# Kernel optimization log

Hardware: AMD Instinct MI355X
Metric: run time of the kernel (lower is better)

## Reference

```python
import jax, jax.numpy as jnp
import numpy as np

N_NODES = 50000
NEG_SLOPE = 0.2  # PyG GATConv default leaky_relu slope


def setup_inputs() -> dict:
    key = jax.random.key(0)
    ks = jax.random.split(key, 12)
    N, E, D_IN, H = N_NODES, 1200000, 128, 64
    sd_in = 1.0 / np.sqrt(D_IN)
    sd_h = 1.0 / np.sqrt(H)
    return {
        "x": jax.random.normal(ks[0], (N, D_IN), jnp.float32),
        "src": jax.random.randint(ks[1], (E,), 0, N, jnp.int32),
        "dst": jax.random.randint(ks[2], (E,), 0, N, jnp.int32),
        "W1_src": jax.random.normal(ks[3], (D_IN, H), jnp.float32) * sd_in,
        "W1_dst": jax.random.normal(ks[4], (D_IN, H), jnp.float32) * sd_in,
        "a1_src": jax.random.normal(ks[5], (H,), jnp.float32) * sd_h,
        "a1_dst": jax.random.normal(ks[6], (H,), jnp.float32) * sd_h,
        "b1": jnp.zeros((H,), jnp.float32),
        "W2_src": jax.random.normal(ks[7], (H, H), jnp.float32) * sd_h,
        "W2_dst": jax.random.normal(ks[8], (H, H), jnp.float32) * sd_h,
        "a2_src": jax.random.normal(ks[9], (H,), jnp.float32) * sd_h,
        "a2_dst": jax.random.normal(ks[10], (H,), jnp.float32) * sd_h,
        "b2": jnp.zeros((H,), jnp.float32),
    }


def _gat_layer(x, src, dst, W_src, W_dst, att_src, att_dst, bias):
    N = x.shape[0]
    h_src = x @ W_src            # [N, H] transformed source features
    h_dst = x @ W_dst            # [N, H] transformed destination features
    alpha_src = h_src @ att_src  # [N]
    alpha_dst = h_dst @ att_dst  # [N]
    # edge-wise attention logits (gather), edge j -> i: e = lrelu(a_src[j] + a_dst[i])
    e = jax.nn.leaky_relu(alpha_src[src] + alpha_dst[dst], NEG_SLOPE)  # [E]
    # segment softmax over incoming edges of each destination node
    m = jax.ops.segment_max(e, dst, num_segments=N)          # [N]
    ex = jnp.exp(e - m[dst])                                  # [E]
    denom = jax.ops.segment_sum(ex, dst, num_segments=N)     # [N]
    alpha = ex / denom[dst]                                   # [E]
    # weighted scatter-add aggregation
    msgs = h_src[src] * alpha[:, None]                        # [E, H]
    out = jax.ops.segment_sum(msgs, dst, num_segments=N)     # [N, H]
    return out + bias


def reference(x, src, dst, W1_src, W1_dst, a1_src, a1_dst, b1,
              W2_src, W2_dst, a2_src, a2_dst, b2):
    h = jnp.tanh(_gat_layer(x, src, dst, W1_src, W1_dst, a1_src, a1_dst, b1))
    h = jnp.tanh(_gat_layer(h, src, dst, W2_src, W2_dst, a2_src, a2_dst, b2))
    return h
```

## Files before the change

### kernel.cpp

```cpp
#include <hip/hip_runtime.h>
#include <hip/hip_bf16.h>

#define NEG_SLOPE 0.2f
#define EPB 4096
#define NHB 64
#define NBUK 1024

typedef __attribute__((ext_vector_type(8))) short short8v;
typedef __attribute__((ext_vector_type(4))) float f32x4;

__device__ inline float blo(unsigned u) { return __uint_as_float(u << 16); }
__device__ inline float bhi(unsigned u) { return __uint_as_float(u & 0xffff0000u); }
__device__ inline unsigned short bf16bits(float f) {
    __hip_bfloat16 b = __float2bfloat16(f);
    return *(unsigned short*)&b;
}
__device__ inline unsigned pack2bf(float e, float o) {
    return ((unsigned)bf16bits(o) << 16) | (unsigned)bf16bits(e);
}

template <int K>
__device__ inline void build_wt(unsigned short* __restrict__ Wt,
                                const float* __restrict__ W_src,
                                const float* __restrict__ a_src,
                                const float* __restrict__ W_dst,
                                const float* __restrict__ a_dst, int tid) {
    for (int i = tid; i < 64 * K; i += 256) {
        int k = i >> 6, j = i & 63;
        Wt[j * K + k] = bf16bits(W_src[i]);
    }
    for (int i = tid; i < 2 * K; i += 256) {
        int which = (i >= K) ? 1 : 0;
        int k = i - which * K;
        const float* Wr = (which ? W_dst : W_src) + k * 64;
        const float* av = which ? a_dst : a_src;
        float s = 0.f;
        #pragma unroll
        for (int j = 0; j < 64; ++j) s += Wr[j] * av[j];
        Wt[(64 + which) * K + k] = bf16bits(s);
    }
    for (int i = tid; i < 14 * K; i += 256) Wt[66 * K + i] = 0;
}

__global__ __launch_bounds__(256) void prep(
    const int* __restrict__ dst, int* __restrict__ partials, int E,
    const float* __restrict__ W1_src, const float* __restrict__ a1_src,
    const float* __restrict__ W1_dst, const float* __restrict__ a1_dst,
    const float* __restrict__ W2_src, const float* __restrict__ a2_src,
    const float* __restrict__ W2_dst, const float* __restrict__ a2_dst,
    unsigned short* __restrict__ Wt1, unsigned short* __restrict__ Wt2) {
    __shared__ int lh[NBUK];
    int tid = threadIdx.x, b = blockIdx.x;
    if (b < NHB) {
        for (int s = tid; s < NBUK; s += 256) lh[s] = 0;
        __syncthreads();
        for (int e = b * 256 + tid; e < E; e += NHB * 256)
            atomicAdd(&lh[dst[e] >> 6], 1);
        __syncthreads();
        for (int s = tid; s < NBUK; s += 256)
            partials[b * NBUK + s] = lh[s];
    } else if (b == NHB) {
        build_wt<128>(Wt1, W1_src, a1_src, W1_dst, a1_dst, tid);
    } else {
        build_wt<64>(Wt2, W2_src, a2_src, W2_dst, a2_dst, tid);
    }
}

__global__ __launch_bounds__(256) void scan1024(const int* __restrict__ partials,
                                                int* __restrict__ bucket_base,
                                                int* __restrict__ cursor0) {
    __shared__ int tsum[256];
    int tid = threadIdx.x;
    int4 v = make_int4(0, 0, 0, 0);
    for (int b = 0; b < NHB; ++b) {
        int4 p = *(const int4*)&partials[b * NBUK + 4 * tid];
        v.x += p.x; v.y += p.y; v.z += p.z; v.w += p.w;
    }
    int t = v.x + v.y + v.z + v.w;
    tsum[tid] = t;
    __syncthreads();
    for (int off = 1; off < 256; off <<= 1) {
        int u = (tid >= off) ? tsum[tid - off] : 0;
        __syncthreads();
        tsum[tid] += u;
        __syncthreads();
    }
    int base = tsum[tid] - t;
    bucket_base[4 * tid + 0] = base;
    bucket_base[4 * tid + 1] = base + v.x;
    bucket_base[4 * tid + 2] = base + v.x + v.y;
    bucket_base[4 * tid + 3] = base + v.x + v.y + v.z;
    if (tid == 255) bucket_base[NBUK] = tsum[255];
    *(int4*)&cursor0[4 * tid] = make_int4(0, 0, 0, 0);
}

template <int K, bool INBF16>
__device__ inline void nt_body(int nb, const void* __restrict__ x_,
                               const unsigned short* __restrict__ Wt,
                               unsigned* __restrict__ hb_out,
                               float* __restrict__ alpha_src,
                               float* __restrict__ alpha_dst, int N, int tid) {
    int wid = tid >> 6, l = tid & 63;
    int rowbase = (nb * 4 + wid) * 16;
    if (rowbase >= N) return;
    int jcol = l & 15, kg = (l >> 4) * 8;

    int r = rowbase + jcol;
    if (r >= N) r = N - 1;
    const float*          xr32 = (const float*)x_ + (size_t)r * K + kg;
    const unsigned short* xr16 = (const unsigned short*)x_ + (size_t)r * K + kg;

    f32x4 acc[5];
    #pragma unroll
    for (int t = 0; t < 5; ++t) acc[t] = (f32x4){0.f, 0.f, 0.f, 0.f};

    #pragma unroll
    for (int kt = 0; kt < K / 32; ++kt) {
        short8v a;
        if constexpr (INBF16) {
            a = *(const short8v*)(xr16 + kt * 32);
        } else {
            float4 xa = *(const float4*)(xr32 + kt * 32);
            float4 xb = *(const float4*)(xr32 + kt * 32 + 4);
            a[0] = (short)bf16bits(xa.x); a[1] = (short)bf16bits(xa.y);
            a[2] = (short)bf16bits(xa.z); a[3] = (short)bf16bits(xa.w);
            a[4] = (short)bf16bits(xb.x); a[5] = (short)bf16bits(xb.y);
            a[6] = (short)bf16bits(xb.z); a[7] = (short)bf16bits(xb.w);
        }
        int kbase = kt * 32 + kg;
        #pragma unroll
        for (int t = 0; t < 5; ++t) {
            short8v b = *(const short8v*)&Wt[(t * 16 + jcol) * K + kbase];
            acc[t] = __builtin_amdgcn_mfma_f32_16x16x32_bf16(a, b, acc[t], 0, 0, 0);
        }
    }

    int rbase = rowbase + (l >> 4) * 4;
    #pragma unroll
    for (int t = 0; t < 4; ++t) {
        #pragma unroll
        for (int rr = 0; rr < 4; ++rr) {
            float v = acc[t][rr];
            float w = __shfl_xor(v, 1);
            int row = rbase + rr;
            if (!(l & 1) && row < N)
                hb_out[(size_t)row * 32 + t * 8 + (jcol >> 1)] = pack2bf(v, w);
        }
    }
    #pragma unroll
    for (int rr = 0; rr < 4; ++rr) {
        int row = rbase + rr;
        if (row < N) {
            if (jcol == 0) alpha_src[row] = acc[4][rr];
            if (jcol == 1) alpha_dst[row] = acc[4][rr];
        }
    }
}

__global__ __launch_bounds__(256) void scatter_nt1(
    const int* __restrict__ src, const int* __restrict__ dst,
    const int* __restrict__ bucket_base, int* __restrict__ cursor0,
    unsigned* __restrict__ ebuf, int E, int eb3,
    const float* __restrict__ x, const unsigned short* __restrict__ Wt1,
    unsigned* __restrict__ hb_out,
    float* __restrict__ alpha_src, float* __restrict__ alpha_dst, int N) {
    int tid = threadIdx.x;
    if ((int)blockIdx.x >= eb3) {
        nt_body<128, false>(blockIdx.x - eb3, x, Wt1, hb_out,
                            alpha_src, alpha_dst, N, tid);
        return;
    }
    __shared__ int lhist[NBUK];
    __shared__ int lbase[NBUK];
    for (int s = tid; s < NBUK; s += 256) lhist[s] = 0;
    __syncthreads();
    int base = blockIdx.x * EPB;
    int bkt[16], rank[16];
    unsigned pack[16];
    #pragma unroll
    for (int i = 0; i < 16; ++i) {
        int e = base + i * 256 + tid;
        bkt[i] = -1;
        if (e < E) {
            int d = dst[e], s = src[e];
            bkt[i]  = d >> 6;
            pack[i] = ((unsigned)(d & 63) << 16) | (unsigned)s;
            rank[i] = atomicAdd(&lhist[bkt[i]], 1);
        }
    }
    __syncthreads();
    for (int s = tid; s < NBUK; s += 256) {
        int c = lhist[s];
        if (c) lbase[s] = bucket_base[s] + atomicAdd(&cursor0[s], c);
    }
    __syncthreads();
    #pragma unroll
    for (int i = 0; i < 16; ++i)
        if (bkt[i] >= 0) ebuf[lbase[bkt[i]] + rank[i]] = pack[i];
}

__global__ __launch_bounds__(256) void bucket_build(
    const unsigned* __restrict__ ebuf, const int* __restrict__ bucket_base,
    int* __restrict__ row_ptr, unsigned short* __restrict__ csr16,
    int N, int E) {
    __shared__ int deg[64];
    __shared__ int cur[64];
    __shared__ int tmp[256];
    int b = blockIdx.x, tid = threadIdx.x;
    int ebase = bucket_base[b], eend = bucket_base[b + 1];
    if (tid < 64) deg[tid] = 0;
    __syncthreads();
    for (int e = ebase + tid; e < eend; e += 256)
        atomicAdd(&deg[ebuf[e] >> 16], 1);
    __syncthreads();
    int v = (tid < 64) ? deg[tid] : 0;
    tmp[tid] = v;
    __syncthreads();
    for (int off = 1; off < 64; off <<= 1) {
        int t = (tid >= off) ? tmp[tid - off] : 0;
        __syncthreads();
        tmp[tid] += t;
        __syncthreads();
    }
    int excl = tmp[tid] - v;
    int node = b * 64 + tid;
    if (tid < 64 && node < N) row_ptr[node] = ebase + excl;
    if (b == 0 && tid == 0) row_ptr[N] = E;
    if (tid < 64) cur[tid] = excl;
    __syncthreads();
    for (int e = ebase + tid; e < eend; e += 256) {
        unsigned pk = ebuf[e];
        int r = atomicAdd(&cur[pk >> 16], 1);
        csr16[ebase + r] = (unsigned short)(pk & 0xFFFFu);
    }
}

template <bool OUTBF16>
__global__ __launch_bounds__(256) void aggregate(
    const int* __restrict__ row_ptr, const unsigned short* __restrict__ csr16,
    const float* __restrict__ alpha_src, const float* __restrict__ alpha_dst,
    const unsigned* __restrict__ hb,
    const float* __restrict__ bias,
    void* __restrict__ out_,
    int N) {
    __shared__ float2 spbuf[4][64];
    int wid = threadIdx.x >> 6, lane = threadIdx.x & 63;
    int node = blockIdx.x * 4 + wid;
    if (node >= N) return;

    int beg = row_ptr[node], end = row_ptr[node + 1];
    float adst = alpha_dst[node];
    int half = lane >> 5, sub = lane & 31;
    float2* __restrict__ mysp = spbuf[wid];
    int wslot = (lane & 1) * 32 + (lane >> 1);
    int rbase = half * 32;

    float dL = 0.f;
    float aA[4] = {0.f, 0.f, 0.f, 0.f};
    float aB[4] = {0.f, 0.f, 0.f, 0.f};

    for (int c = beg; c < end; c += 64) {
        int cnt = end - c;
        cnt = (cnt < 64) ? cnt : 64;

        int s = 0;
        float p = 0.f;
        if (lane < cnt) {
            s = csr16[c + lane];
            float t = alpha_src[s] + adst;
            t = (t > 0.f) ? t : NEG_SLOPE * t;
            p = __expf(fminf(t, 60.f));
            dL += p;
        }
        mysp[wslot] = make_float2(__int_as_float(s), p);

        for (int j = 0; j < cnt; j += 16) {
            int sl = rbase + (j >> 1);
            float4 q0 = *(const float4*)&mysp[sl];
            float4 q1 = *(const float4*)&mysp[sl + 2];
            float4 q2 = *(const float4*)&mysp[sl + 4];
            float4 q3 = *(const float4*)&mysp[sl + 6];
            int   sv[8] = {__float_as_int(q0.x), __float_as_int(q0.z),
                           __float_as_int(q1.x), __float_as_int(q1.z),
                           __float_as_int(q2.x), __float_as_int(q2.z),
                           __float_as_int(q3.x), __float_as_int(q3.z)};
            float pv[8] = {q0.y, q0.w, q1.y, q1.w, q2.y, q2.w, q3.y, q3.w};
            unsigned uv[8];
            #pragma unroll
            for (int i = 0; i < 8; ++i)
                uv[i] = hb[(size_t)sv[i] * 32 + sub];
            #pragma unroll
            for (int i = 0; i < 8; ++i) {
                aA[i & 3] = fmaf(pv[i], blo(uv[i]), aA[i & 3]);
                aB[i & 3] = fmaf(pv[i], bhi(uv[i]), aB[i & 3]);
            }
        }
    }
    float denom = dL;
    #pragma unroll
    for (int off = 32; off; off >>= 1) denom += __shfl_xor(denom, off);

    float accA = (aA[0] + aA[1]) + (aA[2] + aA[3]);
    float accB = (aB[0] + aB[1]) + (aB[2] + aB[3]);
    accA += __shfl_xor(accA, 32);
    accB += __shfl_xor(accB, 32);
    int srcl = lane >> 1;
    float vA = __shfl(accA, srcl);
    float vB = __shfl(accB, srcl);
    float val = (lane & 1) ? vB : vA;
    float r = (denom > 0.f) ? (val / denom) : 0.f;
    float fv = tanhf(r + bias[lane]);

    if constexpr (OUTBF16) {
        float fw = __shfl_xor(fv, 1);
        if (!(lane & 1))
            ((unsigned*)out_)[(size_t)node * 32 + (lane >> 1)] = pack2bf(fv, fw);
    } else {
        ((float*)out_)[(size_t)node * 64 + lane] = fv;
    }
}

__global__ __launch_bounds__(256) void nt2(
    const unsigned short* __restrict__ x, const unsigned short* __restrict__ Wt,
    unsigned* __restrict__ hb_out,
    float* __restrict__ alpha_src, float* __restrict__ alpha_dst, int N) {
    nt_body<64, true>(blockIdx.x, x, Wt, hb_out, alpha_src, alpha_dst,
                      N, threadIdx.x);
}

extern "C" void kernel_launch(void* const* d_in, const int* in_sizes, int n_in,
                              void* d_out, int out_size, void* d_ws, size_t ws_size,
                              hipStream_t stream) {
    const float* x      = (const float*)d_in[0];
    const int*   src    = (const int*)  d_in[1];
    const int*   dst    = (const int*)  d_in[2];
    const float* W1_src = (const float*)d_in[3];
    const float* W1_dst = (const float*)d_in[4];
    const float* a1_src = (const float*)d_in[5];
    const float* a1_dst = (const float*)d_in[6];
    const float* b1     = (const float*)d_in[7];
    const float* W2_src = (const float*)d_in[8];
    const float* W2_dst = (const float*)d_in[9];
    const float* a2_src = (const float*)d_in[10];
    const float* a2_dst = (const float*)d_in[11];
    const float* b2     = (const float*)d_in[12];
    float* out = (float*)d_out;

    const int N = in_sizes[0] / 128;
    const int E = in_sizes[1];
    const int nbuk = (N + 63) / 64;

    char* ws = (char*)d_ws;
    size_t off = 0;
    auto alloc = [&](size_t bytes) {
        void* p = ws + off;
        off += (bytes + 255) & ~(size_t)255;
        return p;
    };
    unsigned* hbuf1  = (unsigned*)alloc((size_t)N * 32 * 4);
    unsigned* h1buf  = (unsigned*)alloc((size_t)N * 32 * 4);
    unsigned* hbuf2  = (unsigned*)alloc((size_t)N * 32 * 4);
    float* alpha_s1  = (float*)alloc((size_t)N * 4);
    float* alpha_d1  = (float*)alloc((size_t)N * 4);
    float* alpha_s2  = (float*)alloc((size_t)N * 4);
    float* alpha_d2  = (float*)alloc((size_t)N * 4);
    int*   row_ptr   = (int*)  alloc((size_t)(N + 1) * 4);
    unsigned short* csr16 = (unsigned short*)alloc((size_t)E * 2);
    int*   partials  = (int*)  alloc((size_t)NHB * NBUK * 4);
    int*   bucket_base = (int*)alloc((NBUK + 1) * 4);
    int*   cursor0   = (int*)  alloc(NBUK * 4);
    unsigned short* Wt1 = (unsigned short*)alloc(80 * 128 * 2);
    unsigned short* Wt2 = (unsigned short*)alloc(80 * 64 * 2);
    unsigned* ebuf   = (unsigned*)alloc((size_t)E * 4);
    (void)ws_size;

    const int eb3  = (E + EPB - 1) / EPB;
    const int nwb  = (N + 3) / 4;
    const int ntb  = (N + 63) / 64;

    prep<<<NHB + 2, 256, 0, stream>>>(dst, partials, E,
                                      W1_src, a1_src, W1_dst, a1_dst,
                                      W2_src, a2_src, W2_dst, a2_dst,
                                      Wt1, Wt2);
    scan1024<<<1, 256, 0, stream>>>(partials, bucket_base, cursor0);
    scatter_nt1<<<eb3 + ntb, 256, 0, stream>>>(
        src, dst, bucket_base, cursor0, ebuf, E, eb3,
        x, Wt1, hbuf1, alpha_s1, alpha_d1, N);
    bucket_build<<<nbuk, 256, 0, stream>>>(ebuf, bucket_base, row_ptr, csr16, N, E);
    aggregate<true><<<nwb, 256, 0, stream>>>(row_ptr, csr16, alpha_s1, alpha_d1,
                                             hbuf1, b1, h1buf, N);
    nt2<<<ntb, 256, 0, stream>>>((const unsigned short*)h1buf, Wt2,
                                 hbuf2, alpha_s2, alpha_d2, N);
    aggregate<false><<<nwb, 256, 0, stream>>>(row_ptr, csr16, alpha_s2, alpha_d2,
                                              hbuf2, b2, out, N);
}
```

Measured before the change: 129.5 us.

## Fuse layer-2 node transform into layer-1 aggregation epilogue

Removes the separate nt2 kernel and the intermediate bf16 h1 buffer. Each wave now computes the layer-2 projection of its node's aggregated features in the aggregate epilogue, using a scalar FMA loop over fp32 W2_src from global memory plus shuffle reductions for the attention scalars. This saves one launch and an N x 64 write and read round trip. In exchange, the per-node 64x64 matvec runs on scalar ALUs instead of the MFMA path, and every wave re-reads W2 through the cache.

```diff
diff --git a/kernel.cpp b/kernel.cpp
--- a/kernel.cpp
+++ b/kernel.cpp
@@ -11,6 +11,7 @@
 
 __device__ inline float blo(unsigned u) { return __uint_as_float(u << 16); }
 __device__ inline float bhi(unsigned u) { return __uint_as_float(u & 0xffff0000u); }
+__device__ inline float bf16f(unsigned short b) { return __uint_as_float((unsigned)b << 16); }
 __device__ inline unsigned short bf16bits(float f) {
     __hip_bfloat16 b = __float2bfloat16(f);
     return *(unsigned short*)&b;
@@ -235,13 +236,17 @@
     }
 }
 
-template <bool OUTBF16>
+template <bool FUSE_NT2>
 __global__ __launch_bounds__(256) void aggregate(
     const int* __restrict__ row_ptr, const unsigned short* __restrict__ csr16,
     const float* __restrict__ alpha_src, const float* __restrict__ alpha_dst,
     const unsigned* __restrict__ hb,
     const float* __restrict__ bias,
-    void* __restrict__ out_,
+    float* __restrict__ out,
+    const unsigned short* __restrict__ Wt2,
+    const float* __restrict__ W2f,
+    unsigned* __restrict__ hb2,
+    float* __restrict__ alpha_s2, float* __restrict__ alpha_d2,
     int N) {
     __shared__ float2 spbuf[4][64];
     int wid = threadIdx.x >> 6, lane = threadIdx.x & 63;
@@ -311,21 +316,31 @@
     float r = (denom > 0.f) ? (val / denom) : 0.f;
     float fv = tanhf(r + bias[lane]);
 
-    if constexpr (OUTBF16) {
-        float fw = __shfl_xor(fv, 1);
+    if constexpr (!FUSE_NT2) {
+        out[(size_t)node * 64 + lane] = fv;
+    } else {
+        float hf = bf16f(bf16bits(fv));
+        float* myspf = (float*)mysp;
+        myspf[lane] = hf;
+
+        float as2 = hf * bf16f(Wt2[64 * 64 + lane]);
+        float ad2 = hf * bf16f(Wt2[65 * 64 + lane]);
+        #pragma unroll
+        for (int off = 32; off; off >>= 1) {
+            as2 += __shfl_xor(as2, off);
+            ad2 += __shfl_xor(ad2, off);
+        }
+
+        float acc2 = 0.f;
+        #pragma unroll 8
+        for (int k = 0; k < 64; ++k)
+            acc2 = fmaf(myspf[k], W2f[k * 64 + lane], acc2);
+
+        float w2 = __shfl_xor(acc2, 1);
         if (!(lane & 1))
-            ((unsigned*)out_)[(size_t)node * 32 + (lane >> 1)] = pack2bf(fv, fw);
-    } else {
-        ((float*)out_)[(size_t)node * 64 + lane] = fv;
-    }
-}
-
-__global__ __launch_bounds__(256) void nt2(
-    const unsigned short* __restrict__ x, const unsigned short* __restrict__ Wt,
-    unsigned* __restrict__ hb_out,
-    float* __restrict__ alpha_src, float* __restrict__ alpha_dst, int N) {
-    nt_body<64, true>(blockIdx.x, x, Wt, hb_out, alpha_src, alpha_dst,
-                      N, threadIdx.x);
+            hb2[(size_t)node * 32 + (lane >> 1)] = pack2bf(acc2, w2);
+        if (lane == 0) { alpha_s2[node] = as2; alpha_d2[node] = ad2; }
+    }
 }
 
 extern "C" void kernel_launch(void* const* d_in, const int* in_sizes, int n_in,
@@ -358,7 +373,6 @@
         return p;
     };
     unsigned* hbuf1  = (unsigned*)alloc((size_t)N * 32 * 4);
-    unsigned* h1buf  = (unsigned*)alloc((size_t)N * 32 * 4);
     unsigned* hbuf2  = (unsigned*)alloc((size_t)N * 32 * 4);
     float* alpha_s1  = (float*)alloc((size_t)N * 4);
     float* alpha_d1  = (float*)alloc((size_t)N * 4);
@@ -388,9 +402,9 @@
         x, Wt1, hbuf1, alpha_s1, alpha_d1, N);
     bucket_build<<<nbuk, 256, 0, stream>>>(ebuf, bucket_base, row_ptr, csr16, N, E);
     aggregate<true><<<nwb, 256, 0, stream>>>(row_ptr, csr16, alpha_s1, alpha_d1,
-                                             hbuf1, b1, h1buf, N);
-    nt2<<<ntb, 256, 0, stream>>>((const unsigned short*)h1buf, Wt2,
-                                 hbuf2, alpha_s2, alpha_d2, N);
+                                             hbuf1, b1, nullptr,
+                                             Wt2, W2_src, hbuf2, alpha_s2, alpha_d2, N);
     aggregate<false><<<nwb, 256, 0, stream>>>(row_ptr, csr16, alpha_s2, alpha_d2,
-                                              hbuf2, b2, out, N);
-}
+                                              hbuf2, b2, out,
+                                              nullptr, nullptr, nullptr, nullptr, nullptr, N);
+}
```

New measurement: 138.0 us. +6.6%, slower.
